# Performance work log

Hardware: AMD Instinct MI355X
Metric: run time of the kernel (lower is better)

## Reference

```python
import jax, jax.numpy as jnp
import numpy as np

D, B, E, O = 16, 8, 2048, 2048  # delays, batch, pre, post


def setup_inputs() -> dict:
    key = jax.random.key(0)
    k1, k2, k3, k4, k5, k6 = jax.random.split(key, 6)
    # Sparse nonnegative connectivity scaled by wmax (here wmax=1)
    conn = (jax.random.uniform(k1, (E, O)) < 0.2).astype(jnp.float32)
    W = jax.random.uniform(k2, (E, O), dtype=jnp.float32) * conn
    # align_signs: per-presynaptic-neuron sign in {-1,+1}, zeroed where W<=0
    signs_pre = jnp.where(jax.random.uniform(k3, (E,)) < 0.8, 1.0, -1.0)
    signs = jnp.where(W > 0, signs_pre[:, None], 0.0).astype(jnp.float32)
    Xd = (jax.random.uniform(k4, (D, B, E)) < 0.05).astype(jnp.float32)
    # STP module output (before the +1 applied in forward)
    Wshort = 0.1 * jax.random.normal(k5, (D, B, E), dtype=jnp.float32)
    # delaymap: binary routing mask (delay, pre, post)
    delaymap = (jax.random.uniform(k6, (D, E, O)) < 0.3).astype(jnp.float32)
    return {"W": W, "signs": signs, "Xd": Xd, "Wshort": Wshort, "delaymap": delaymap}


def reference(W, signs, Xd, Wshort, delaymap):
    # DeltaSynapse.forward, active, has_STDP=False, has_STP=True:
    #   W_eff = signs * W                      (e, o)
    #   Wshort_mod = shortterm(Xd) + 1         (d, b, e)
    #   I = einsum('eo,dbe,deo,dbe->bo', W_eff, Xd, delaymap, Wshort_mod)
    Weff = signs * W
    I = jnp.einsum('eo,dbe,deo,dbe->bo', Weff, Xd, delaymap, Wshort + 1.0)
    return I
```

## Files before the change

### kernel.cpp

```cpp
#include <hip/hip_runtime.h>
#include <cstdint>
#include <cstddef>

#define DD 16
#define BB 8
#define EE 2048
#define OO 2048
#define NCH 256

__global__ void pack_coeffs(const float* __restrict__ Xd,
                            const float* __restrict__ Ws,
                            float* __restrict__ Cpack,
                            unsigned* __restrict__ mask) {
    int i = blockIdx.x * 256 + threadIdx.x;
    if (i >= DD * BB * EE) return;
    int e  = i & (EE - 1);
    int db = i >> 11;
    int d  = db >> 3;
    int b  = db & 7;
    float x = Xd[i];
    float v = x * (Ws[i] + 1.0f);
    Cpack[((size_t)e * DD + d) * BB + b] = v;
    if (v != 0.0f) atomicOr(&mask[e], 1u << d);
}

__device__ __forceinline__ void fma4(float4& a, const float4& x, float s) {
    a.x = fmaf(x.x, s, a.x);
    a.y = fmaf(x.y, s, a.y);
    a.z = fmaf(x.z, s, a.z);
    a.w = fmaf(x.w, s, a.w);
}

template <bool USE_PART>
__global__ __launch_bounds__(256, 6)
void synapse_main(const float* __restrict__ W,
                  const float* __restrict__ S,
                  const float* __restrict__ DM,
                  const float* __restrict__ Cpack,
                  const unsigned* __restrict__ mask,
                  float* __restrict__ Pout) {
    const int ot   = blockIdx.x;
    const int ch   = blockIdx.y;
    const int wave = threadIdx.x >> 6;
    const int lane = threadIdx.x & 63;
    const int o0   = ot * 256 + lane * 4;

    float4 acc[BB];
#pragma unroll
    for (int b = 0; b < BB; ++b) acc[b] = make_float4(0.f, 0.f, 0.f, 0.f);

#pragma unroll
    for (int ei = 0; ei < 2; ++ei) {
        const int e = ch * 8 + wave * 2 + ei;

        float4 w4 = *reinterpret_cast<const float4*>(W + (size_t)e * OO + o0);
        float4 s4 = *reinterpret_cast<const float4*>(S + (size_t)e * OO + o0);
        float4 wf;
        wf.x = w4.x * s4.x; wf.y = w4.y * s4.y;
        wf.z = w4.z * s4.z; wf.w = w4.w * s4.w;

        unsigned m = mask[e];
        while (m) {
            const int d = __builtin_ctz(m);
            m &= (m - 1);
            const float4* cp = reinterpret_cast<const float4*>(
                Cpack + ((size_t)e * DD + d) * BB);
            float4 c0 = cp[0];
            float4 c1 = cp[1];
            float4 dm = *reinterpret_cast<const float4*>(
                DM + ((size_t)d * EE + e) * OO + o0);
            float4 dw;
            dw.x = dm.x * wf.x; dw.y = dm.y * wf.y;
            dw.z = dm.z * wf.z; dw.w = dm.w * wf.w;
            fma4(acc[0], dw, c0.x); fma4(acc[1], dw, c0.y);
            fma4(acc[2], dw, c0.z); fma4(acc[3], dw, c0.w);
            fma4(acc[4], dw, c1.x); fma4(acc[5], dw, c1.y);
            fma4(acc[6], dw, c1.z); fma4(acc[7], dw, c1.w);
        }
    }

    __shared__ __align__(16) float red[4][4][256];
    const int t = threadIdx.x;
#pragma unroll
    for (int p = 0; p < 2; ++p) {
#pragma unroll
        for (int bb = 0; bb < 4; ++bb)
            *reinterpret_cast<float4*>(&red[wave][bb][lane * 4]) = acc[p * 4 + bb];
        __syncthreads();
        if (USE_PART) {
#pragma unroll
            for (int bb = 0; bb < 4; ++bb) {
                float s = red[0][bb][t] + red[1][bb][t] +
                          red[2][bb][t] + red[3][bb][t];
                Pout[((size_t)ch * BB + (p * 4 + bb)) * OO + ot * 256 + t] = s;
            }
        } else {
#pragma unroll
            for (int bb = 0; bb < 4; ++bb) {
                float s = red[0][bb][t] + red[1][bb][t] +
                          red[2][bb][t] + red[3][bb][t];
                atomicAdd(Pout + (size_t)(p * 4 + bb) * OO + ot * 256 + t, s);
            }
        }
        __syncthreads();
    }
}

__global__ void reduce_partials(const float* __restrict__ P,
                                float* __restrict__ out) {
    int i = blockIdx.x * 256 + threadIdx.x;
    if (i >= BB * OO) return;
    int b = i >> 11;
    int o = i & (OO - 1);
    float s0 = 0.f, s1 = 0.f, s2 = 0.f, s3 = 0.f;
    const float* p = P + (size_t)b * OO + o;
#pragma unroll 4
    for (int ch = 0; ch < NCH; ch += 4) {
        s0 += p[(size_t)(ch + 0) * BB * OO];
        s1 += p[(size_t)(ch + 1) * BB * OO];
        s2 += p[(size_t)(ch + 2) * BB * OO];
        s3 += p[(size_t)(ch + 3) * BB * OO];
    }
    out[(size_t)b * OO + o] = (s0 + s1) + (s2 + s3);
}

__global__ __launch_bounds__(256, 6)
void synapse_nows(const float* __restrict__ W,
                  const float* __restrict__ S,
                  const float* __restrict__ Xd,
                  const float* __restrict__ Ws,
                  const float* __restrict__ DM,
                  float* __restrict__ out) {
    const int ot   = blockIdx.x;
    const int ch   = blockIdx.y;
    const int wave = threadIdx.x >> 6;
    const int lane = threadIdx.x & 63;
    const int o0   = ot * 256 + lane * 4;

    float4 acc[BB];
#pragma unroll
    for (int b = 0; b < BB; ++b) acc[b] = make_float4(0.f, 0.f, 0.f, 0.f);

#pragma unroll
    for (int ei = 0; ei < 2; ++ei) {
        const int e = ch * 8 + wave * 2 + ei;

        float4 w4 = *reinterpret_cast<const float4*>(W + (size_t)e * OO + o0);
        float4 s4 = *reinterpret_cast<const float4*>(S + (size_t)e * OO + o0);
        float4 wf;
        wf.x = w4.x * s4.x; wf.y = w4.y * s4.y;
        wf.z = w4.z * s4.z; wf.w = w4.w * s4.w;

        for (int d = 0; d < DD; ++d) {
            float c[BB];
            bool nz = false;
#pragma unroll
            for (int b = 0; b < BB; ++b) {
                size_t idx = (size_t)(d * BB + b) * EE + e;
                float x = Xd[idx];
                c[b] = x * (Ws[idx] + 1.0f);
                nz |= (c[b] != 0.f);
            }
            if (!nz) continue;
            float4 dm = *reinterpret_cast<const float4*>(
                DM + ((size_t)d * EE + e) * OO + o0);
            float4 dw;
            dw.x = dm.x * wf.x; dw.y = dm.y * wf.y;
            dw.z = dm.z * wf.z; dw.w = dm.w * wf.w;
#pragma unroll
            for (int b = 0; b < BB; ++b) fma4(acc[b], dw, c[b]);
        }
    }

    __shared__ __align__(16) float red[4][4][256];
    const int t = threadIdx.x;
#pragma unroll
    for (int p = 0; p < 2; ++p) {
#pragma unroll
        for (int bb = 0; bb < 4; ++bb)
            *reinterpret_cast<float4*>(&red[wave][bb][lane * 4]) = acc[p * 4 + bb];
        __syncthreads();
#pragma unroll
        for (int bb = 0; bb < 4; ++bb) {
            float s = red[0][bb][t] + red[1][bb][t] +
                      red[2][bb][t] + red[3][bb][t];
            atomicAdd(out + (size_t)(p * 4 + bb) * OO + ot * 256 + t, s);
        }
        __syncthreads();
    }
}

extern "C" void kernel_launch(void* const* d_in, const int* in_sizes, int n_in,
                              void* d_out, int out_size, void* d_ws, size_t ws_size,
                              hipStream_t stream) {
    const float* W  = (const float*)d_in[0];
    const float* S  = (const float*)d_in[1];
    const float* Xd = (const float*)d_in[2];
    const float* Ws = (const float*)d_in[3];
    const float* DM = (const float*)d_in[4];
    float* out = (float*)d_out;

    const size_t packBytes = (size_t)EE * DD * BB * sizeof(float);
    const size_t maskBytes = (size_t)EE * sizeof(unsigned);
    const size_t partBytes = (size_t)NCH * BB * OO * sizeof(float);

    char* ws = (char*)d_ws;
    const bool canPack = ws_size >= packBytes + maskBytes;
    const bool canPart = ws_size >= packBytes + maskBytes + partBytes;

    dim3 grid(8, NCH), blk(256);

    if (canPack) {
        float*    Cp = (float*)ws;
        unsigned* mk = (unsigned*)(ws + packBytes);
        hipMemsetAsync(mk, 0, maskBytes, stream);
        pack_coeffs<<<(DD * BB * EE + 255) / 256, 256, 0, stream>>>(Xd, Ws, Cp, mk);
        if (canPart) {
            float* P = (float*)(ws + packBytes + maskBytes);
            synapse_main<true><<<grid, blk, 0, stream>>>(W, S, DM, Cp, mk, P);
            reduce_partials<<<(BB * OO + 255) / 256, 256, 0, stream>>>(P, out);
        } else {
            hipMemsetAsync(out, 0, (size_t)BB * OO * sizeof(float), stream);
            synapse_main<false><<<grid, blk, 0, stream>>>(W, S, DM, Cp, mk, out);
        }
    } else {
        hipMemsetAsync(out, 0, (size_t)BB * OO * sizeof(float), stream);
        synapse_nows<<<grid, blk, 0, stream>>>(W, S, Xd, Ws, DM, out);
    }
}
```

Baseline: 377.7 us.

## Interleave two presynaptic rows per wave and replace partial-sum reduction with atomics

The main kernel now walks the delay masks of both presynaptic rows in one loop, issuing both rows' coefficient and delaymap loads before the FMAs so more memory requests are in flight per wave. The per-chunk partial buffer and its separate reduction kernel are dropped in favour of float atomicAdd into the output, which is now zeroed inside the pack kernel rather than by a memset. Launch bounds drop from 6 to 4 waves per SIMD, allowing more registers for the doubled loads but lowering occupancy. Atomic contention across 256 chunks per output element could become a new cost.

```diff
diff --git a/kernel.cpp b/kernel.cpp
--- a/kernel.cpp
+++ b/kernel.cpp
@@ -11,8 +11,10 @@
 __global__ void pack_coeffs(const float* __restrict__ Xd,
                             const float* __restrict__ Ws,
                             float* __restrict__ Cpack,
-                            unsigned* __restrict__ mask) {
+                            unsigned* __restrict__ mask,
+                            float* __restrict__ out) {
     int i = blockIdx.x * 256 + threadIdx.x;
+    if (i < BB * OO) out[i] = 0.0f;
     if (i >= DD * BB * EE) return;
     int e  = i & (EE - 1);
     int db = i >> 11;
@@ -31,51 +33,79 @@
     a.w = fmaf(x.w, s, a.w);
 }
 
-template <bool USE_PART>
-__global__ __launch_bounds__(256, 6)
+__global__ __launch_bounds__(256, 4)
 void synapse_main(const float* __restrict__ W,
                   const float* __restrict__ S,
                   const float* __restrict__ DM,
                   const float* __restrict__ Cpack,
                   const unsigned* __restrict__ mask,
-                  float* __restrict__ Pout) {
+                  float* __restrict__ out) {
     const int ot   = blockIdx.x;
     const int ch   = blockIdx.y;
     const int wave = threadIdx.x >> 6;
     const int lane = threadIdx.x & 63;
     const int o0   = ot * 256 + lane * 4;
+    const int e0   = ch * 8 + wave * 2;
+    const int e1   = e0 + 1;
 
     float4 acc[BB];
 #pragma unroll
     for (int b = 0; b < BB; ++b) acc[b] = make_float4(0.f, 0.f, 0.f, 0.f);
 
-#pragma unroll
-    for (int ei = 0; ei < 2; ++ei) {
-        const int e = ch * 8 + wave * 2 + ei;
-
-        float4 w4 = *reinterpret_cast<const float4*>(W + (size_t)e * OO + o0);
-        float4 s4 = *reinterpret_cast<const float4*>(S + (size_t)e * OO + o0);
-        float4 wf;
-        wf.x = w4.x * s4.x; wf.y = w4.y * s4.y;
-        wf.z = w4.z * s4.z; wf.w = w4.w * s4.w;
-
-        unsigned m = mask[e];
-        while (m) {
-            const int d = __builtin_ctz(m);
-            m &= (m - 1);
+    float4 w0 = *reinterpret_cast<const float4*>(W + (size_t)e0 * OO + o0);
+    float4 s0 = *reinterpret_cast<const float4*>(S + (size_t)e0 * OO + o0);
+    float4 w1 = *reinterpret_cast<const float4*>(W + (size_t)e1 * OO + o0);
+    float4 s1 = *reinterpret_cast<const float4*>(S + (size_t)e1 * OO + o0);
+    float4 wf0, wf1;
+    wf0.x = w0.x * s0.x; wf0.y = w0.y * s0.y;
+    wf0.z = w0.z * s0.z; wf0.w = w0.w * s0.w;
+    wf1.x = w1.x * s1.x; wf1.y = w1.y * s1.y;
+    wf1.z = w1.z * s1.z; wf1.w = w1.w * s1.w;
+
+    unsigned m0 = mask[e0];
+    unsigned m1 = mask[e1];
+
+    while (m0 | m1) {
+        const unsigned a0 = m0, a1 = m1;
+        float4 c00, c01, dm0;
+        float4 c10, c11, dm1;
+        if (a0) {
+            const int d = __builtin_ctz(m0);
+            m0 &= (m0 - 1);
             const float4* cp = reinterpret_cast<const float4*>(
-                Cpack + ((size_t)e * DD + d) * BB);
-            float4 c0 = cp[0];
-            float4 c1 = cp[1];
-            float4 dm = *reinterpret_cast<const float4*>(
-                DM + ((size_t)d * EE + e) * OO + o0);
+                Cpack + ((size_t)e0 * DD + d) * BB);
+            c00 = cp[0];
+            c01 = cp[1];
+            dm0 = *reinterpret_cast<const float4*>(
+                DM + ((size_t)d * EE + e0) * OO + o0);
+        }
+        if (a1) {
+            const int d = __builtin_ctz(m1);
+            m1 &= (m1 - 1);
+            const float4* cp = reinterpret_cast<const float4*>(
+                Cpack + ((size_t)e1 * DD + d) * BB);
+            c10 = cp[0];
+            c11 = cp[1];
+            dm1 = *reinterpret_cast<const float4*>(
+                DM + ((size_t)d * EE + e1) * OO + o0);
+        }
+        if (a0) {
             float4 dw;
-            dw.x = dm.x * wf.x; dw.y = dm.y * wf.y;
-            dw.z = dm.z * wf.z; dw.w = dm.w * wf.w;
-            fma4(acc[0], dw, c0.x); fma4(acc[1], dw, c0.y);
-            fma4(acc[2], dw, c0.z); fma4(acc[3], dw, c0.w);
-            fma4(acc[4], dw, c1.x); fma4(acc[5], dw, c1.y);
-            fma4(acc[6], dw, c1.z); fma4(acc[7], dw, c1.w);
+            dw.x = dm0.x * wf0.x; dw.y = dm0.y * wf0.y;
+            dw.z = dm0.z * wf0.z; dw.w = dm0.w * wf0.w;
+            fma4(acc[0], dw, c00.x); fma4(acc[1], dw, c00.y);
+            fma4(acc[2], dw, c00.z); fma4(acc[3], dw, c00.w);
+            fma4(acc[4], dw, c01.x); fma4(acc[5], dw, c01.y);
+            fma4(acc[6], dw, c01.z); fma4(acc[7], dw, c01.w);
+        }
+        if (a1) {
+            float4 dw;
+            dw.x = dm1.x * wf1.x; dw.y = dm1.y * wf1.y;
+            dw.z = dm1.z * wf1.z; dw.w = dm1.w * wf1.w;
+            fma4(acc[0], dw, c10.x); fma4(acc[1], dw, c10.y);
+            fma4(acc[2], dw, c10.z); fma4(acc[3], dw, c10.w);
+            fma4(acc[4], dw, c11.x); fma4(acc[5], dw, c11.y);
+            fma4(acc[6], dw, c11.z); fma4(acc[7], dw, c11.w);
         }
     }
 
@@ -87,44 +117,17 @@
         for (int bb = 0; bb < 4; ++bb)
             *reinterpret_cast<float4*>(&red[wave][bb][lane * 4]) = acc[p * 4 + bb];
         __syncthreads();
-        if (USE_PART) {
-#pragma unroll
-            for (int bb = 0; bb < 4; ++bb) {
-                float s = red[0][bb][t] + red[1][bb][t] +
-                          red[2][bb][t] + red[3][bb][t];
-                Pout[((size_t)ch * BB + (p * 4 + bb)) * OO + ot * 256 + t] = s;
-            }
-        } else {
-#pragma unroll
-            for (int bb = 0; bb < 4; ++bb) {
-                float s = red[0][bb][t] + red[1][bb][t] +
-                          red[2][bb][t] + red[3][bb][t];
-                atomicAdd(Pout + (size_t)(p * 4 + bb) * OO + ot * 256 + t, s);
-            }
-        }
-        __syncthreads();
-    }
-}
-
-__global__ void reduce_partials(const float* __restrict__ P,
-                                float* __restrict__ out) {
-    int i = blockIdx.x * 256 + threadIdx.x;
-    if (i >= BB * OO) return;
-    int b = i >> 11;
-    int o = i & (OO - 1);
-    float s0 = 0.f, s1 = 0.f, s2 = 0.f, s3 = 0.f;
-    const float* p = P + (size_t)b * OO + o;
-#pragma unroll 4
-    for (int ch = 0; ch < NCH; ch += 4) {
-        s0 += p[(size_t)(ch + 0) * BB * OO];
-        s1 += p[(size_t)(ch + 1) * BB * OO];
-        s2 += p[(size_t)(ch + 2) * BB * OO];
-        s3 += p[(size_t)(ch + 3) * BB * OO];
-    }
-    out[(size_t)b * OO + o] = (s0 + s1) + (s2 + s3);
-}
-
-__global__ __launch_bounds__(256, 6)
+#pragma unroll
+        for (int bb = 0; bb < 4; ++bb) {
+            float s = red[0][bb][t] + red[1][bb][t] +
+                      red[2][bb][t] + red[3][bb][t];
+            atomicAdd(out + (size_t)(p * 4 + bb) * OO + ot * 256 + t, s);
+        }
+        __syncthreads();
+    }
+}
+
+__global__ __launch_bounds__(256, 4)
 void synapse_nows(const float* __restrict__ W,
                   const float* __restrict__ S,
                   const float* __restrict__ Xd,
@@ -190,6 +193,11 @@
     }
 }
 
+__global__ void zero_out(float* __restrict__ out) {
+    int i = blockIdx.x * 256 + threadIdx.x;
+    if (i < BB * OO) out[i] = 0.0f;
+}
+
 extern "C" void kernel_launch(void* const* d_in, const int* in_sizes, int n_in,
                               void* d_out, int out_size, void* d_ws, size_t ws_size,
                               hipStream_t stream) {
@@ -202,11 +210,9 @@
 
     const size_t packBytes = (size_t)EE * DD * BB * sizeof(float);
     const size_t maskBytes = (size_t)EE * sizeof(unsigned);
-    const size_t partBytes = (size_t)NCH * BB * OO * sizeof(float);
 
     char* ws = (char*)d_ws;
     const bool canPack = ws_size >= packBytes + maskBytes;
-    const bool canPart = ws_size >= packBytes + maskBytes + partBytes;
 
     dim3 grid(8, NCH), blk(256);
 
@@ -214,17 +220,10 @@
         float*    Cp = (float*)ws;
         unsigned* mk = (unsigned*)(ws + packBytes);
         hipMemsetAsync(mk, 0, maskBytes, stream);
-        pack_coeffs<<<(DD * BB * EE + 255) / 256, 256, 0, stream>>>(Xd, Ws, Cp, mk);
-        if (canPart) {
-            float* P = (float*)(ws + packBytes + maskBytes);
-            synapse_main<true><<<grid, blk, 0, stream>>>(W, S, DM, Cp, mk, P);
-            reduce_partials<<<(BB * OO + 255) / 256, 256, 0, stream>>>(P, out);
-        } else {
-            hipMemsetAsync(out, 0, (size_t)BB * OO * sizeof(float), stream);
-            synapse_main<false><<<grid, blk, 0, stream>>>(W, S, DM, Cp, mk, out);
-        }
+        pack_coeffs<<<(DD * BB * EE + 255) / 256, 256, 0, stream>>>(Xd, Ws, Cp, mk, out);
+        synapse_main<<<grid, blk, 0, stream>>>(W, S, DM, Cp, mk, out);
     } else {
-        hipMemsetAsync(out, 0, (size_t)BB * OO * sizeof(float), stream);
+        zero_out<<<(BB * OO + 255) / 256, 256, 0, stream>>>(out);
         synapse_nows<<<grid, blk, 0, stream>>>(W, S, Xd, Ws, DM, out);
     }
 }
```

Result: faster. 353.1 us (-6.5%).
